# Kernel tuning notes

Measured on AMD Instinct MI355X. Metric: run time of the kernel, lower is better.

The kernel has to match this reference:

```python
import jax, jax.numpy as jnp
import numpy as np

N, IN_C, OUT_C, H, CF = 4096, 256, 256, 8, 6
D = OUT_C // H

def setup_inputs() -> dict:
    key = jax.random.key(0)
    ks = jax.random.split(key, 8)
    x = jax.random.normal(ks[0], (N, IN_C), dtype=jnp.float32)
    positions = jax.random.normal(ks[1], (N, 3), dtype=jnp.float32)
    curv_feats = jax.random.normal(ks[2], (N, CF), dtype=jnp.float32)
    adj = jax.random.randint(ks[3], (N, N), 0, 2, dtype=jnp.int32)
    W = jax.random.normal(ks[4], (OUT_C, IN_C), dtype=jnp.float32) * 0.05
    a_l = jax.random.normal(ks[5], (H, D), dtype=jnp.float32) * 0.1
    a_r = jax.random.normal(ks[6], (H, D), dtype=jnp.float32) * 0.1
    Wc = jax.random.normal(ks[7], (H, CF), dtype=jnp.float32) * 0.1
    gate = jnp.asarray(0.1, dtype=jnp.float32)
    return {"x": x, "positions": positions, "curv_feats": curv_feats,
            "adj": adj, "W": W, "a_l": a_l, "a_r": a_r, "Wc": Wc, "gate": gate}

def reference(x, positions, curv_feats, adj, W, a_l, a_r, Wc, gate):
    n = x.shape[0]
    h = (x @ W.T).reshape(n, H, D)                       # (N,H,D)
    e_l = jnp.einsum('nhd,hd->nh', h, a_l)               # (N,H)
    e_r = jnp.einsum('nhd,hd->nh', h, a_r)               # (N,H)
    logits = jax.nn.leaky_relu(e_l[:, None, :] + e_r[None, :, :], negative_slope=0.2)  # (N,N,H)
    curv_pair = jnp.abs(curv_feats[:, None, :] - curv_feats[None, :, :])  # (N,N,CF)
    curv_bias = jnp.einsum('ijf,hf->ijh', curv_pair, Wc)                  # (N,N,H)
    logits = logits + gate * curv_bias
    mask = (adj > 0)[:, :, None]                          # (N,N,1)
    logits = jnp.where(mask, logits, jnp.float32(-1e9))
    attn = jax.nn.softmax(logits, axis=1)                 # softmax over j (dim=1)
    out = jnp.einsum('ijh,jhd->ihd', attn, h)             # (N,H,D)
    return out.reshape(n, H * D)
```

## Files before the change

kernel.cpp:

```cpp
#include <hip/hip_runtime.h>

#define NN 4096
#define HC 8
#define DC 32
#define OC 256
#define KC 256
#define CF 6

typedef _Float16 f16_t;
typedef f16_t f16x2 __attribute__((ext_vector_type(2)));
typedef f16_t f16x8 __attribute__((ext_vector_type(8)));
typedef float f32x4 __attribute__((ext_vector_type(4)));
typedef float f32x2 __attribute__((ext_vector_type(2)));
typedef unsigned u32x4 __attribute__((ext_vector_type(4)));

union HU { f16x2 h; unsigned u; };

extern "C" __device__ _Float16 __ocml_exp2_f16(_Float16);

__global__ __launch_bounds__(256) void prep_all(const float* __restrict__ x,
                                                const float* __restrict__ W,
                                                const float* __restrict__ a_l,
                                                const float* __restrict__ a_r,
                                                const int* __restrict__ adj,
                                                const float* __restrict__ cfeat,
                                                const float* __restrict__ Wc,
                                                const float* __restrict__ gate,
                                                float* __restrict__ e_l2,
                                                f16_t* __restrict__ erP,
                                                f16_t* __restrict__ hT2,
                                                unsigned* __restrict__ adjb,
                                                float* __restrict__ cfT,
                                                f16_t* __restrict__ cfP,
                                                float* __restrict__ Wc2) {
  __shared__ float As[16][68];
  __shared__ float Bs[16][36];
  __shared__ float Ct[DC][65];
  const float LOG2E = 1.44269504088896340736f;
  const int t = threadIdx.x;
  const int bid = blockIdx.x;

  if (bid >= 512) {
    const int pb = bid - 512;
    const int ptid = pb * 256 + t;
    const int lane = t & 63;
    const int wv = pb * 4 + (t >> 6);
    int v[32];
#pragma unroll
    for (int u = 0; u < 32; ++u) {
      int g = wv * 32 + u;
      v[u] = adj[(size_t)(g >> 6) * NN + (g & 63) * 64 + lane];
    }
#pragma unroll
    for (int u = 0; u < 32; ++u) {
      int g = wv * 32 + u;
      unsigned long long m = __ballot(v[u] > 0);
      if (lane == 0) *(unsigned long long*)(adjb + (g >> 6) * 128 + (g & 63) * 2) = m;
    }
    if (ptid < NN * CF) {
      int j = ptid / CF, f = ptid - j * CF;
      float vv = cfeat[ptid];
      cfT[f * NN + j] = vv;
      int cc = j >> 5, qq = (j >> 3) & 3, tt = j & 7;
      cfP[((cc * 4 + qq) * CF + f) * 8 + tt] = (f16_t)vv;
    }
    if (ptid < HC * CF) Wc2[ptid] = Wc[ptid] * gate[0] * LOG2E;
    return;
  }

  const int i0 = (bid & 63) * 64;
  const int head = bid >> 6;
  const int c0 = head * DC;
  const int tx = t & 7;
  const int ty = t >> 3;
  const int lr = t >> 2;
  const int lk = (t & 3) * 4;

  float acc[2][4] = {};
  f32x4 av = *(const f32x4*)&x[(size_t)(i0 + lr) * KC + lk];
  f32x4 wv = {};
  if (t < 128) wv = *(const f32x4*)&W[(size_t)(c0 + (t >> 2)) * KC + lk];
  for (int kk = 0; kk < KC; kk += 16) {
    __syncthreads();
    As[lk + 0][lr] = av[0]; As[lk + 1][lr] = av[1];
    As[lk + 2][lr] = av[2]; As[lk + 3][lr] = av[3];
    if (t < 128) {
      int br = t >> 2;
      Bs[lk + 0][br] = wv[0]; Bs[lk + 1][br] = wv[1];
      Bs[lk + 2][br] = wv[2]; Bs[lk + 3][br] = wv[3];
    }
    __syncthreads();
    if (kk + 16 < KC) {
      av = *(const f32x4*)&x[(size_t)(i0 + lr) * KC + kk + 16 + lk];
      if (t < 128) wv = *(const f32x4*)&W[(size_t)(c0 + (t >> 2)) * KC + kk + 16 + lk];
    }
#pragma unroll
    for (int k = 0; k < 16; ++k) {
      f32x2 a = *(const f32x2*)&As[k][ty * 2];
      f32x4 b = *(const f32x4*)&Bs[k][tx * 4];
#pragma unroll
      for (int r = 0; r < 2; ++r)
#pragma unroll
        for (int u = 0; u < 4; ++u)
          acc[r][u] += a[r] * b[u];
    }
  }

  f32x4 al4 = *(const f32x4*)&a_l[c0 + tx * 4];
  f32x4 ar4 = *(const f32x4*)&a_r[c0 + tx * 4];
#pragma unroll
  for (int r = 0; r < 2; ++r) {
    float el = acc[r][0] * al4[0] + acc[r][1] * al4[1] +
               acc[r][2] * al4[2] + acc[r][3] * al4[3];
    float er = acc[r][0] * ar4[0] + acc[r][1] * ar4[1] +
               acc[r][2] * ar4[2] + acc[r][3] * ar4[3];
    el += __shfl_xor(el, 1, 64); el += __shfl_xor(el, 2, 64); el += __shfl_xor(el, 4, 64);
    er += __shfl_xor(er, 1, 64); er += __shfl_xor(er, 2, 64); er += __shfl_xor(er, 4, 64);
    if (tx == 0) {
      int j = i0 + ty * 2 + r;
      e_l2[j * HC + head] = el * LOG2E;
      int cc = j >> 5, qq = (j >> 3) & 3, tt = j & 7;
      erP[((cc * 4 + qq) * HC + head) * 8 + tt] = (f16_t)(er * LOG2E);
    }
  }

#pragma unroll
  for (int r = 0; r < 2; ++r)
#pragma unroll
    for (int u = 0; u < 4; ++u)
      Ct[tx * 4 + u][ty * 2 + r] = acc[r][u];
  __syncthreads();
  const size_t base = (size_t)head * (NN / 32) * 1024 + (size_t)(bid & 63) * 2048;
#pragma unroll
  for (int rep = 0; rep < 8; ++rep) {
    int idx = rep * 256 + t;
    int dd = (idx >> 3) & 31;
    int jl = (idx >> 10) * 32 + ((idx >> 8) & 3) * 8 + (idx & 7);
    hT2[base + idx] = (f16_t)Ct[dd][jl];
  }
}

__global__ __launch_bounds__(256, 4) void attn(const unsigned* __restrict__ adjb,
                                               const float* __restrict__ e_l2,
                                               const float* __restrict__ cfT,
                                               const float* __restrict__ Wc2,
                                               const u32x4* __restrict__ cfP4,
                                               const u32x4* __restrict__ erP4,
                                               const f16_t* __restrict__ hT2,
                                               float* __restrict__ Sws,
                                               float* __restrict__ out) {
  __shared__ float Obuf[16][64];
  __shared__ float Sbuf[16][2];
  const int tid = threadIdx.x;
  const int w = tid >> 6;
  const int lane = tid & 63;
  const int il = lane & 15;
  const int quad = lane >> 4;
  const int ibase = blockIdx.x * 16;
  const int hg = blockIdx.y;
  const int cbase = blockIdx.z * 64;
  const int i = ibase + il;

  for (int idx = tid; idx < 16 * 64; idx += 256) (&Obuf[0][0])[idx] = 0.f;
  if (tid < 32) (&Sbuf[0][0])[tid] = 0.f;
  __syncthreads();

  f16x2 cfi2h[CF];
#pragma unroll
  for (int f = 0; f < CF; ++f) {
    f16_t v = (f16_t)cfT[f * NN + i];
    cfi2h[f] = (f16x2){v, v};
  }
  f16x2 elh[2];
  {
    f32x2 e0 = *(const f32x2*)&e_l2[i * HC + hg * 2];
#pragma unroll
    for (int u = 0; u < 2; ++u) { f16_t v = (f16_t)e0[u]; elh[u] = (f16x2){v, v}; }
  }
  f16x2 wch[2][CF];
#pragma unroll
  for (int h = 0; h < 2; ++h)
#pragma unroll
    for (int f = 0; f < CF; ++f) {
      f16_t v = (f16_t)Wc2[(hg * 2 + h) * CF + f];
      wch[h][f] = (f16x2){v, v};
    }
  const f16x2 lslope = (f16x2){(f16_t)0.2f, (f16_t)0.2f};
  const f16x8 onesB = {(f16_t)1.f, (f16_t)1.f, (f16_t)1.f, (f16_t)1.f,
                       (f16_t)1.f, (f16_t)1.f, (f16_t)1.f, (f16_t)1.f};

  f32x4 acc[2][2];
#pragma unroll
  for (int h = 0; h < 2; ++h)
#pragma unroll
    for (int d = 0; d < 2; ++d) acc[h][d] = (f32x4){0.f, 0.f, 0.f, 0.f};
  f32x4 Sacc[2];
#pragma unroll
  for (int h = 0; h < 2; ++h) Sacc[h] = (f32x4){0.f, 0.f, 0.f, 0.f};

  const f16_t* hTbase = hT2 + (size_t)hg * 2 * ((NN / 32) * 1024) + quad * 256 + il * 8;
  const u32x4* cfb = cfP4 + quad * CF;
  const u32x4* erb = erP4 + quad * HC + hg * 2;
  const unsigned* adjrow = adjb + i * 128;

  u32x4 cfc[CF];
#pragma unroll
  for (int f = 0; f < CF; ++f) cfc[f] = cfb[(cbase + w) * (4 * CF) + f];
  u32x4 erc[2];
#pragma unroll
  for (int h = 0; h < 2; ++h) erc[h] = erb[(cbase + w) * (4 * HC) + h];
  unsigned mc = adjrow[cbase + w];

#pragma unroll 2
  for (int c = cbase + w; c < cbase + 64; c += 4) {
    const f16_t* bp0 = hTbase + c * 1024;
    const f16_t* bp1 = bp0 + (NN / 32) * 1024;
    f16x8 b00 = *(const f16x8*)bp0;
    f16x8 b01 = *(const f16x8*)(bp0 + 128);
    f16x8 b10 = *(const f16x8*)bp1;
    f16x8 b11 = *(const f16x8*)(bp1 + 128);

    const unsigned m8 = (mc >> (quad * 8)) & 0xffu;

    f16x2 arg[2][4];
#pragma unroll
    for (int p = 0; p < 4; ++p) {
      HU mb;
      mb.u = (((m8 >> (2 * p)) & 1u) ? 0u : 0xFC00u) |
             (((m8 >> (2 * p + 1)) & 1u) ? 0u : 0xFC000000u);
      f16x2 bias0 = mb.h;
      f16x2 bias1 = mb.h;
#pragma unroll
      for (int f = 0; f < CF; ++f) {
        HU cu; cu.u = cfc[f][p];
        f16x2 d = cfi2h[f] - cu.h;
        f16x2 ad = __builtin_elementwise_max(d, -d);
        bias0 = __builtin_elementwise_fma(ad, wch[0][f], bias0);
        bias1 = __builtin_elementwise_fma(ad, wch[1][f], bias1);
      }
#pragma unroll
      for (int h = 0; h < 2; ++h) {
        HU eu; eu.u = erc[h][p];
        f16x2 s = elh[h] + eu.h;
        f16x2 lk = __builtin_elementwise_max(s, lslope * s);
        arg[h][p] = lk + (h ? bias1 : bias0);
      }
    }

    {
      const int cn = cbase + ((c - cbase + 4) & 63);
#pragma unroll
      for (int f = 0; f < CF; ++f) cfc[f] = cfb[cn * (4 * CF) + f];
#pragma unroll
      for (int h = 0; h < 2; ++h) erc[h] = erb[cn * (4 * HC) + h];
      mc = adjrow[cn];
    }

    union { f16x8 v; unsigned u[4]; } af[2];
#pragma unroll
    for (int p = 0; p < 4; ++p) {
#pragma unroll
      for (int h = 0; h < 2; ++h) {
        f16x2 a = arg[h][p];
        f16x2 r;
        r[0] = __ocml_exp2_f16(a[0]);
        r[1] = __ocml_exp2_f16(a[1]);
        HU pu; pu.h = r;
        af[h].u[p] = pu.u;
      }
    }

#pragma unroll
    for (int h = 0; h < 2; ++h) {
      acc[h][0] = __builtin_amdgcn_mfma_f32_16x16x32_f16(af[h].v, h ? b10 : b00, acc[h][0], 0, 0, 0);
      acc[h][1] = __builtin_amdgcn_mfma_f32_16x16x32_f16(af[h].v, h ? b11 : b01, acc[h][1], 0, 0, 0);
      Sacc[h] = __builtin_amdgcn_mfma_f32_16x16x32_f16(af[h].v, onesB, Sacc[h], 0, 0, 0);
    }
  }

  if (il == 0) {
#pragma unroll
    for (int h = 0; h < 2; ++h)
#pragma unroll
      for (int r = 0; r < 4; ++r)
        atomicAdd(&Sbuf[quad * 4 + r][h], Sacc[h][r]);
  }
#pragma unroll
  for (int h = 0; h < 2; ++h)
#pragma unroll
    for (int dh = 0; dh < 2; ++dh)
#pragma unroll
      for (int r = 0; r < 4; ++r)
        atomicAdd(&Obuf[quad * 4 + r][h * DC + dh * 16 + il], acc[h][dh][r]);
  __syncthreads();

  if (tid < 32) {
    int row = tid >> 1, h = tid & 1;
    atomicAdd(&Sws[(size_t)(ibase + row) * HC + hg * 2 + h], Sbuf[row][h]);
  }
  for (int idx = tid; idx < 16 * 64; idx += 256) {
    int row = idx >> 6;
    int colg = idx & 63;
    atomicAdd(&out[(size_t)(ibase + row) * OC + hg * 64 + colg], Obuf[row][colg]);
  }
}

__global__ __launch_bounds__(256) void divS(const float* __restrict__ Sws,
                                            float* __restrict__ out) {
  const int idx = blockIdx.x * 256 + threadIdx.x;
  const int i = idx >> 6;
  const int c4 = idx & 63;
  const int head = c4 >> 3;
  f32x4 v = ((f32x4*)out)[idx];
  const float s = Sws[i * HC + head];
  ((f32x4*)out)[idx] = v / s;
}

extern "C" void kernel_launch(void* const* d_in, const int* in_sizes, int n_in,
                              void* d_out, int out_size, void* d_ws, size_t ws_size,
                              hipStream_t stream) {
  const float* x    = (const float*)d_in[0];
  const float* cfeat= (const float*)d_in[2];
  const int*   adj  = (const int*)d_in[3];
  const float* W    = (const float*)d_in[4];
  const float* a_l  = (const float*)d_in[5];
  const float* a_r  = (const float*)d_in[6];
  const float* Wc   = (const float*)d_in[7];
  const float* gate = (const float*)d_in[8];
  float* out = (float*)d_out;

  char* ws = (char*)d_ws;
  f16_t*    hT2  = (f16_t*)ws;
  unsigned* adjb = (unsigned*)(ws + (2u << 20));
  float*    e_l2 = (float*)(ws + (4u << 20));
  float*    cfT  = (float*)(ws + (4u << 20) + (128u << 10));
  float*    Wc2  = (float*)(ws + (4u << 20) + (256u << 10));
  f16_t*    cfP  = (f16_t*)(ws + (4u << 20) + (320u << 10));
  f16_t*    erP  = (f16_t*)(ws + (4u << 20) + (384u << 10));
  float*    Sws  = (float*)(ws + (4u << 20) + (448u << 10));

  hipMemsetAsync(out, 0, (size_t)NN * OC * sizeof(float), stream);
  hipMemsetAsync(Sws, 0, (size_t)NN * HC * sizeof(float), stream);
  prep_all<<<2560, 256, 0, stream>>>(x, W, a_l, a_r, adj, cfeat, Wc, gate,
                                     e_l2, erP, hT2, adjb, cfT, cfP, Wc2);
  attn<<<dim3(NN / 16, 4, 2), 256, 0, stream>>>(adjb, e_l2, cfT, Wc2,
                                                (const u32x4*)cfP,
                                                (const u32x4*)erP,
                                                hT2, Sws, out);
  divS<<<(NN * OC / 4) / 256, 256, 0, stream>>>(Sws, out);
}
```

Measured before the change: 211.2 us.

## Replace ones-MFMA row sums with fdot2, drop memsets and global atomics

New measurement: 208.1 us. About the same (-1.5%).

```diff
diff --git a/kernel.cpp b/kernel.cpp
--- a/kernel.cpp
+++ b/kernel.cpp
@@ -10,11 +10,13 @@
 typedef _Float16 f16_t;
 typedef f16_t f16x2 __attribute__((ext_vector_type(2)));
 typedef f16_t f16x8 __attribute__((ext_vector_type(8)));
+typedef __fp16 hh2 __attribute__((ext_vector_type(2)));
 typedef float f32x4 __attribute__((ext_vector_type(4)));
 typedef float f32x2 __attribute__((ext_vector_type(2)));
 typedef unsigned u32x4 __attribute__((ext_vector_type(4)));
 
 union HU { f16x2 h; unsigned u; };
+union HW { hh2 r; unsigned u; };
 
 extern "C" __device__ _Float16 __ocml_exp2_f16(_Float16);
 
@@ -140,14 +142,16 @@
   }
 }
 
-__global__ __launch_bounds__(256, 4) void attn(const unsigned* __restrict__ adjb,
+__global__ __launch_bounds__(256, 5) void attn(const unsigned* __restrict__ adjb,
                                                const float* __restrict__ e_l2,
                                                const float* __restrict__ cfT,
                                                const float* __restrict__ Wc2,
                                                const u32x4* __restrict__ cfP4,
                                                const u32x4* __restrict__ erP4,
                                                const f16_t* __restrict__ hT2,
-                                               float* __restrict__ Sws,
+                                               float* __restrict__ Sws0,
+                                               float* __restrict__ Sws1,
+                                               float* __restrict__ outP,
                                                float* __restrict__ out) {
   __shared__ float Obuf[16][64];
   __shared__ float Sbuf[16][2];
@@ -186,17 +190,13 @@
       wch[h][f] = (f16x2){v, v};
     }
   const f16x2 lslope = (f16x2){(f16_t)0.2f, (f16_t)0.2f};
-  const f16x8 onesB = {(f16_t)1.f, (f16_t)1.f, (f16_t)1.f, (f16_t)1.f,
-                       (f16_t)1.f, (f16_t)1.f, (f16_t)1.f, (f16_t)1.f};
 
   f32x4 acc[2][2];
 #pragma unroll
   for (int h = 0; h < 2; ++h)
 #pragma unroll
     for (int d = 0; d < 2; ++d) acc[h][d] = (f32x4){0.f, 0.f, 0.f, 0.f};
-  f32x4 Sacc[2];
-#pragma unroll
-  for (int h = 0; h < 2; ++h) Sacc[h] = (f32x4){0.f, 0.f, 0.f, 0.f};
+  float S[2] = {0.f, 0.f};
 
   const f16_t* hTbase = hT2 + (size_t)hg * 2 * ((NN / 32) * 1024) + quad * 256 + il * 8;
   const u32x4* cfb = cfP4 + quad * CF;
@@ -267,6 +267,9 @@
         r[1] = __ocml_exp2_f16(a[1]);
         HU pu; pu.h = r;
         af[h].u[p] = pu.u;
+        HW pw; pw.u = pu.u;
+        HW on; on.r = (hh2){(__fp16)1.f, (__fp16)1.f};
+        S[h] = __builtin_amdgcn_fdot2(pw.r, on.r, S[h], false);
       }
     }
 
@@ -274,16 +277,15 @@
     for (int h = 0; h < 2; ++h) {
       acc[h][0] = __builtin_amdgcn_mfma_f32_16x16x32_f16(af[h].v, h ? b10 : b00, acc[h][0], 0, 0, 0);
       acc[h][1] = __builtin_amdgcn_mfma_f32_16x16x32_f16(af[h].v, h ? b11 : b01, acc[h][1], 0, 0, 0);
-      Sacc[h] = __builtin_amdgcn_mfma_f32_16x16x32_f16(af[h].v, onesB, Sacc[h], 0, 0, 0);
-    }
-  }
-
-  if (il == 0) {
-#pragma unroll
-    for (int h = 0; h < 2; ++h)
-#pragma unroll
-      for (int r = 0; r < 4; ++r)
-        atomicAdd(&Sbuf[quad * 4 + r][h], Sacc[h][r]);
+    }
+  }
+
+#pragma unroll
+  for (int h = 0; h < 2; ++h) {
+    float v = S[h];
+    v += __shfl_xor(v, 16, 64);
+    v += __shfl_xor(v, 32, 64);
+    if (quad == 0) atomicAdd(&Sbuf[il][h], v);
   }
 #pragma unroll
   for (int h = 0; h < 2; ++h)
@@ -294,25 +296,29 @@
         atomicAdd(&Obuf[quad * 4 + r][h * DC + dh * 16 + il], acc[h][dh][r]);
   __syncthreads();
 
+  float* So = blockIdx.z ? Sws1 : Sws0;
+  float* Oo = blockIdx.z ? outP : out;
   if (tid < 32) {
     int row = tid >> 1, h = tid & 1;
-    atomicAdd(&Sws[(size_t)(ibase + row) * HC + hg * 2 + h], Sbuf[row][h]);
+    So[(size_t)(ibase + row) * HC + hg * 2 + h] = Sbuf[row][h];
   }
   for (int idx = tid; idx < 16 * 64; idx += 256) {
     int row = idx >> 6;
     int colg = idx & 63;
-    atomicAdd(&out[(size_t)(ibase + row) * OC + hg * 64 + colg], Obuf[row][colg]);
+    Oo[(size_t)(ibase + row) * OC + hg * 64 + colg] = Obuf[row][colg];
   }
 }
 
-__global__ __launch_bounds__(256) void divS(const float* __restrict__ Sws,
+__global__ __launch_bounds__(256) void divS(const float* __restrict__ Sws0,
+                                            const float* __restrict__ Sws1,
+                                            const float* __restrict__ outP,
                                             float* __restrict__ out) {
   const int idx = blockIdx.x * 256 + threadIdx.x;
   const int i = idx >> 6;
   const int c4 = idx & 63;
   const int head = c4 >> 3;
-  f32x4 v = ((f32x4*)out)[idx];
-  const float s = Sws[i * HC + head];
+  f32x4 v = ((const f32x4*)out)[idx] + ((const f32x4*)outP)[idx];
+  const float s = Sws0[i * HC + head] + Sws1[i * HC + head];
   ((f32x4*)out)[idx] = v / s;
 }
 
@@ -337,15 +343,15 @@
   float*    Wc2  = (float*)(ws + (4u << 20) + (256u << 10));
   f16_t*    cfP  = (f16_t*)(ws + (4u << 20) + (320u << 10));
   f16_t*    erP  = (f16_t*)(ws + (4u << 20) + (384u << 10));
-  float*    Sws  = (float*)(ws + (4u << 20) + (448u << 10));
-
-  hipMemsetAsync(out, 0, (size_t)NN * OC * sizeof(float), stream);
-  hipMemsetAsync(Sws, 0, (size_t)NN * HC * sizeof(float), stream);
+  float*    Sws0 = (float*)(ws + (4u << 20) + (448u << 10));
+  float*    Sws1 = (float*)(ws + (4u << 20) + (576u << 10));
+  float*    outP = (float*)(ws + (5u << 20));
+
   prep_all<<<2560, 256, 0, stream>>>(x, W, a_l, a_r, adj, cfeat, Wc, gate,
                                      e_l2, erP, hT2, adjb, cfT, cfP, Wc2);
   attn<<<dim3(NN / 16, 4, 2), 256, 0, stream>>>(adjb, e_l2, cfT, Wc2,
                                                 (const u32x4*)cfP,
                                                 (const u32x4*)erP,
-                                                hT2, Sws, out);
-  divS<<<(NN * OC / 4) / 256, 256, 0, stream>>>(Sws, out);
+                                                hT2, Sws0, Sws1, outP, out);
+  divS<<<(NN * OC / 4) / 256, 256, 0, stream>>>(Sws0, Sws1, outP, out);
 }
```
